# Optimization experiments

Hardware: AMD Instinct MI355X
Metric: run time of the kernel (lower is better)

## Reference

```python
import jax, jax.numpy as jnp
import numpy as np

# Fixed by module source: forward hardcodes a 200x200 BEV grid, dim=128,
# MSDeformAttn(n_levels=1, n_heads=4, n_points=8).
B, Z, X, C, H, P = 2, 200, 200, 128, 4, 8
N = Z * X
D = C // H  # head dim = 32


def setup_inputs() -> dict:
    key = jax.random.key(0)
    ks = jax.random.split(key, 12)
    s = 0.02
    return {
        "query": jax.random.normal(ks[0], (B, N, C), jnp.float32),
        # MSDeformAttn.value_proj
        "Wv": jax.random.normal(ks[1], (C, C), jnp.float32) * s,
        "bv": jnp.zeros((C,), jnp.float32),
        # MSDeformAttn.sampling_offsets (C -> H*1*P*2)
        "Woff": jax.random.normal(ks[2], (C, H * P * 2), jnp.float32) * s,
        "boff": jax.random.normal(ks[3], (H * P * 2,), jnp.float32) * 2.0,
        # MSDeformAttn.attention_weights (C -> H*1*P)
        "Wattn": jax.random.normal(ks[4], (C, H * P), jnp.float32) * s,
        "battn": jnp.zeros((H * P,), jnp.float32),
        # MSDeformAttn.output_proj
        "Wout1": jax.random.normal(ks[5], (C, C), jnp.float32) * s,
        "bout1": jnp.zeros((C,), jnp.float32),
        # VanillaSelfAttention.output_proj
        "Wout2": jax.random.normal(ks[6], (C, C), jnp.float32) * s,
        "bout2": jnp.zeros((C,), jnp.float32),
    }


def _forward(query, Wv, bv, Woff, boff, Wattn, battn, Wout1, bout1, Wout2, bout2):
    # Reference points: normalized centers of the 200x200 grid, order (z, x).
    zc = (jnp.arange(Z, dtype=jnp.float32) + 0.5) / Z
    xc = (jnp.arange(X, dtype=jnp.float32) + 0.5) / X
    ref = jnp.stack(jnp.meshgrid(zc, xc, indexing="ij"), axis=-1).reshape(N, 2)

    # value_proj on input_flatten (== query); split heads, lay out as images.
    value = (query @ Wv + bv).reshape(B, Z, X, H, D)
    value_flat = value.transpose(0, 3, 1, 2, 4).reshape(B * H, Z * X, D)  # (BH, ZX, D)

    # Sampling locations: ref + offsets / offset_normalizer ([W, H] = [200, 200]).
    off = (query @ Woff + boff).reshape(B, N, H, P, 2)
    norm = jnp.array([X, Z], jnp.float32)
    loc = ref[None, :, None, None, :] + off / norm  # (B, N, H, P, 2)

    # Attention weights: softmax over n_levels*n_points (= P here).
    attn = jax.nn.softmax((query @ Wattn + battn).reshape(B, N, H, P), axis=-1)

    # grid_sample convention: grid = 2*loc - 1, grid[...,0]=x (width), align_corners=False.
    grid = 2.0 * loc - 1.0
    ix = ((grid[..., 0] + 1.0) * X - 1.0) * 0.5  # pixel x coords
    iy = ((grid[..., 1] + 1.0) * Z - 1.0) * 0.5  # pixel y coords
    ix = ix.transpose(0, 2, 1, 3).reshape(B * H, N * P)
    iy = iy.transpose(0, 2, 1, 3).reshape(B * H, N * P)

    x0f = jnp.floor(ix); y0f = jnp.floor(iy)
    lx = ix - x0f; ly = iy - y0f
    x0 = x0f.astype(jnp.int32); y0 = y0f.astype(jnp.int32)
    x1 = x0 + 1; y1 = y0 + 1

    def corner(xi, yi, w):
        # zero padding: out-of-bounds corners contribute 0
        valid = (xi >= 0) & (xi < X) & (yi >= 0) & (yi < Z)
        idx = jnp.clip(yi, 0, Z - 1) * X + jnp.clip(xi, 0, X - 1)  # (BH, N*P)
        v = jnp.take_along_axis(value_flat, idx[..., None], axis=1)  # (BH, N*P, D)
        return v * (w * valid.astype(w.dtype))[..., None]

    sampled = (
        corner(x0, y0, (1.0 - lx) * (1.0 - ly))
        + corner(x1, y0, lx * (1.0 - ly))
        + corner(x0, y1, (1.0 - lx) * ly)
        + corner(x1, y1, lx * ly)
    ).reshape(B, H, N, P, D)

    # Weighted reduce over points, merge heads.
    out = jnp.einsum("bhnpd,bnhp->bnhd", sampled, attn).reshape(B, N, C)
    out = out @ Wout1 + bout1  # MSDeformAttn.output_proj
    out = out @ Wout2 + bout2  # VanillaSelfAttention.output_proj
    return out + query  # dropout is identity in eval; residual add


def reference(query, Wv, bv, Woff, boff, Wattn, battn, Wout1, bout1, Wout2, bout2):
    return _forward(query, Wv, bv, Woff, boff, Wattn, battn, Wout1, bout1, Wout2, bout2)
```

## Files before the change

### kernel.cpp

```cpp
#include <hip/hip_runtime.h>
#include <hip/hip_bf16.h>
#include <cstddef>

namespace {
constexpr int B  = 2;
constexpr int Z  = 200;
constexpr int X  = 200;
constexpr int C  = 128;
constexpr int H  = 4;
constexpr int P  = 8;
constexpr int N  = Z * X;
constexpr int BN = B * N;
constexpr int SC = 128;
constexpr int NF_P = 14;
constexpr int NF_O = 8;
constexpr int KS   = 4;

typedef __attribute__((ext_vector_type(8))) short short8;
typedef __attribute__((ext_vector_type(4))) float f32x4;
typedef _Float16 h16x2 __attribute__((ext_vector_type(2)));

__device__ inline ushort f2bf(float x) {
    __hip_bfloat16 h = __float2bfloat16(x);
    return *reinterpret_cast<ushort*>(&h);
}
__device__ inline unsigned packbf(float a, float b) {
    return (unsigned)f2bf(a) | ((unsigned)f2bf(b) << 16);
}
__device__ inline ushort f2h(float x) {
    _Float16 h = (_Float16)x;
    return __builtin_bit_cast(ushort, h);
}
__device__ inline float h1f(ushort u) {
    return (float)__builtin_bit_cast(_Float16, u);
}
__device__ inline float2 h2f2(unsigned u) {
    h16x2 h = __builtin_bit_cast(h16x2, u);
    return make_float2((float)h[0], (float)h[1]);
}
__device__ inline unsigned packh(float a, float b) {
    return (unsigned)f2h(a) | ((unsigned)f2h(b) << 16);
}
__device__ inline h16x2 pkrtz(float a, float b) {
    return __builtin_bit_cast(h16x2, __builtin_amdgcn_cvt_pkrtz(a, b));
}
template <int MASK>
__device__ inline float swzx(float x) {
    constexpr int pat = (MASK << 10) | 0x1F;
    return __int_as_float(__builtin_amdgcn_ds_swizzle(__float_as_int(x), pat));
}
template <int MASK>
__device__ inline h16x2 swzh(h16x2 x) {
    constexpr int pat = (MASK << 10) | 0x1F;
    int t = __builtin_amdgcn_ds_swizzle(__builtin_bit_cast(int, x), pat);
    return __builtin_bit_cast(h16x2, t);
}
}

__global__ __launch_bounds__(256) void vsa_k_prep(
    const float* __restrict__ Wv,    const float* __restrict__ bv,
    const float* __restrict__ Woff,  const float* __restrict__ boff,
    const float* __restrict__ Wattn, const float* __restrict__ battn,
    const float* __restrict__ Wout1, const float* __restrict__ bout1,
    const float* __restrict__ Wout2, const float* __restrict__ bout2,
    ushort* __restrict__ wtp, ushort* __restrict__ wtp2,
    float* __restrict__ biasp, float* __restrict__ bias2)
{
    const int u = blockIdx.x * 256 + threadIdx.x;
    constexpr int NP = KS * NF_P * 64;
    constexpr int NO = KS * NF_O * 64;

    if (u < NP) {
        int ks  = u / (NF_P * 64);
        int rem = u - ks * (NF_P * 64);
        int f = rem >> 6, l = rem & 63;
        int n  = f * 16 + (l & 15);
        int kb = ks * 32 + (l >> 4) * 8;
        float v[8];
        #pragma unroll
        for (int e = 0; e < 8; ++e) {
            int k = kb + e;
            if (n < 128)      v[e] = Wv[k * 128 + n];
            else if (n < 192) v[e] = Woff[k * 64 + (n - 128)];
            else              v[e] = Wattn[k * 32 + (n - 192)];
        }
        unsigned* dst = (unsigned*)(wtp + (size_t)u * 8);
        #pragma unroll
        for (int i = 0; i < 4; ++i) dst[i] = packbf(v[2*i], v[2*i+1]);
    } else if (u < NP + NO) {
        int t   = u - NP;
        int ks  = t / (NF_O * 64);
        int rem = t - ks * (NF_O * 64);
        int f = rem >> 6, l = rem & 63;
        int n  = f * 16 + (l & 15);
        int kb = ks * 32 + (l >> 4) * 8;
        float acc[8] = {0,0,0,0,0,0,0,0};
        for (int j = 0; j < 128; ++j) {
            float w2 = Wout2[j * 128 + n];
            #pragma unroll
            for (int e = 0; e < 8; ++e)
                acc[e] = fmaf(Wout1[(kb + e) * 128 + j], w2, acc[e]);
        }
        unsigned* dst = (unsigned*)(wtp2 + (size_t)t * 8);
        #pragma unroll
        for (int i = 0; i < 4; ++i) dst[i] = packh(acc[2*i], acc[2*i+1]);
    } else if (u < NP + NO + 224) {
        int c = u - NP - NO;
        float bb;
        if (c < 128)      bb = bv[c];
        else if (c < 192) bb = boff[c - 128];
        else              bb = battn[c - 192];
        biasp[c] = bb;
    } else if (u < NP + NO + 224 + 128) {
        int c = u - NP - NO - 224;
        float acc = bout2[c];
        for (int j = 0; j < 128; ++j)
            acc = fmaf(bout1[j], Wout2[j * 128 + c], acc);
        bias2[c] = acc;
    }
}

__global__ __launch_bounds__(256) void vsa_k_proj(
    const float* __restrict__ Q, const ushort* __restrict__ wtp,
    const float* __restrict__ biasp,
    ushort* __restrict__ proj_v16, ushort* __restrict__ proj_s16)
{
    const int lane = threadIdx.x & 63;
    const int wave = blockIdx.x * 4 + (threadIdx.x >> 6);
    const int row0 = wave * 16;
    const int m  = lane & 15;
    const int kg = lane >> 4;

    const float* qp = Q + (size_t)(row0 + m) * 128 + kg * 8;

    f32x4 acc[NF_P];
    #pragma unroll
    for (int f = 0; f < NF_P; ++f) acc[f] = (f32x4){0.f, 0.f, 0.f, 0.f};

    #pragma unroll
    for (int ks = 0; ks < KS; ++ks) {
        float4 a0 = *(const float4*)(qp + ks * 32);
        float4 a1 = *(const float4*)(qp + ks * 32 + 4);
        short8 af;
        af[0] = (short)f2bf(a0.x); af[1] = (short)f2bf(a0.y);
        af[2] = (short)f2bf(a0.z); af[3] = (short)f2bf(a0.w);
        af[4] = (short)f2bf(a1.x); af[5] = (short)f2bf(a1.y);
        af[6] = (short)f2bf(a1.z); af[7] = (short)f2bf(a1.w);
        const short8* wrow = (const short8*)wtp + ks * NF_P * 64 + lane;
        #pragma unroll
        for (int f = 0; f < NF_P; ++f)
            acc[f] = __builtin_amdgcn_mfma_f32_16x16x32_bf16(af, wrow[f * 64], acc[f], 0, 0, 0);
    }

    #pragma unroll
    for (int f = 0; f < 8; ++f) {
        const int col = f * 16 + m;
        const float bb = biasp[col];
        #pragma unroll
        for (int r = 0; r < 4; ++r)
            proj_v16[(size_t)(row0 + kg * 4 + r) * 128 + col] = f2h(acc[f][r] + bb);
    }
    #pragma unroll
    for (int f = 8; f < 12; ++f) {
        const int col = f * 16 + m;
        const float bb = biasp[col];
        const int c  = col - 128;
        const int hp = c >> 1, comp = c & 1;
        #pragma unroll
        for (int r = 0; r < 4; ++r)
            proj_s16[(size_t)(row0 + kg * 4 + r) * SC + hp * 4 + comp] = f2h(acc[f][r] + bb);
    }
    #pragma unroll
    for (int f = 12; f < 14; ++f) {
        const float bb = biasp[f * 16 + m];
        const int hp = (f - 12) * 16 + m;
        #pragma unroll
        for (int r = 0; r < 4; ++r) {
            float v = acc[f][r] + bb;
            float mx = v;
            mx = fmaxf(mx, swzx<1>(mx));
            mx = fmaxf(mx, swzx<2>(mx));
            mx = fmaxf(mx, swzx<4>(mx));
            float ex = __expf(v - mx);
            float sm = ex;
            sm += swzx<1>(sm); sm += swzx<2>(sm); sm += swzx<4>(sm);
            const float wp = ex / sm;
            proj_s16[(size_t)(row0 + kg * 4 + r) * SC + hp * 4 + 2] = f2h(wp);
        }
    }
}

__global__ __launch_bounds__(256) void vsa_k_so(
    const ushort* __restrict__ proj_v16, const ushort* __restrict__ proj_s16,
    const ushort* __restrict__ wtp2, const float* __restrict__ bias2,
    const float* __restrict__ Q, float* __restrict__ out)
{
    __shared__ ushort tmp_lds[16][136];

    const int lane = threadIdx.x & 63;
    const int wv   = threadIdx.x >> 6;
    const int hsub = lane >> 5;
    const int p    = (lane >> 2) & 7;
    const int d8   = lane & 3;

    const int orig = blockIdx.x;
    const int wg   = (orig & 7) * 625 + (orig >> 3);
    const int b    = wg / 2500;
    const int bl0  = (wg - b * 2500) * 16;
    const int i0   = bl0 / 200;
    const int j0   = bl0 - i0 * 200;
    const int bn0  = b * N + bl0;

    const ushort* vb = proj_v16 + (size_t)b * N * 128;

    #pragma unroll
    for (int t = 0; t < 8; ++t) {
        const int unit = t * 4 + wv;
        const int pix  = unit >> 1;
        const int h    = (unit & 1) * 2 + hsub;
        const int jr   = j0 + pix;
        const bool wr  = jr >= 200;
        const int i    = i0 + (wr ? 1 : 0);
        const int j    = wr ? jr - 200 : jr;
        const int bn   = bn0 + pix;

        const uint2 ow = *(const uint2*)(proj_s16 + (size_t)bn * SC + (h * 8 + p) * 4);
        const float2 off = h2f2(ow.x);
        const float  wp  = h1f((ushort)(ow.y & 0xffff));

        const float ixf = (float)i + off.x;
        const float iyf = (float)j + off.y;
        const float x0f = floorf(ixf), y0f = floorf(iyf);
        const float lx = ixf - x0f, ly = iyf - y0f;
        const int x0 = (int)x0f, y0 = (int)y0f;
        const int x1 = x0 + 1,  y1 = y0 + 1;
        const int xc0 = min(max(x0, 0), X - 1), xc1 = min(max(x1, 0), X - 1);
        const int yc0 = min(max(y0, 0), Z - 1), yc1 = min(max(y1, 0), Z - 1);

        const float wx0 = ((unsigned)x0 < (unsigned)X) ? (1.f - lx) : 0.f;
        const float wx1 = ((unsigned)x1 < (unsigned)X) ? lx : 0.f;
        const float wy0 = (((unsigned)y0 < (unsigned)Z) ? (1.f - ly) : 0.f) * wp;
        const float wy1 = (((unsigned)y1 < (unsigned)Z) ? ly : 0.f) * wp;

        const h16x2 w00p = pkrtz(wx0 * wy0, wx0 * wy0);
        const h16x2 w10p = pkrtz(wx1 * wy0, wx1 * wy0);
        const h16x2 w01p = pkrtz(wx0 * wy1, wx0 * wy1);
        const h16x2 w11p = pkrtz(wx1 * wy1, wx1 * wy1);

        const int rb0 = yc0 * X, rb1 = yc1 * X;
        const int hb  = h * 32 + d8 * 8;

        const uint4 c00 = *(const uint4*)(vb + (size_t)(rb0 + xc0) * 128 + hb);
        const uint4 c10 = *(const uint4*)(vb + (size_t)(rb0 + xc1) * 128 + hb);
        const uint4 c01 = *(const uint4*)(vb + (size_t)(rb1 + xc0) * 128 + hb);
        const uint4 c11 = *(const uint4*)(vb + (size_t)(rb1 + xc1) * 128 + hb);

        h16x2 a0 = (h16x2)0, a1 = (h16x2)0, a2 = (h16x2)0, a3 = (h16x2)0;
        #define VSA_ACC(c, wpk) { \
            a0 = __builtin_elementwise_fma(__builtin_bit_cast(h16x2, (c).x), wpk, a0); \
            a1 = __builtin_elementwise_fma(__builtin_bit_cast(h16x2, (c).y), wpk, a1); \
            a2 = __builtin_elementwise_fma(__builtin_bit_cast(h16x2, (c).z), wpk, a2); \
            a3 = __builtin_elementwise_fma(__builtin_bit_cast(h16x2, (c).w), wpk, a3); }
        VSA_ACC(c00, w00p)
        VSA_ACC(c10, w10p)
        VSA_ACC(c01, w01p)
        VSA_ACC(c11, w11p)
        #undef VSA_ACC

        a0 += swzh<4>(a0);  a1 += swzh<4>(a1);  a2 += swzh<4>(a2);  a3 += swzh<4>(a3);
        a0 += swzh<8>(a0);  a1 += swzh<8>(a1);  a2 += swzh<8>(a2);  a3 += swzh<8>(a3);
        a0 += swzh<16>(a0); a1 += swzh<16>(a1); a2 += swzh<16>(a2); a3 += swzh<16>(a3);

        if (p == 0) {
            uint4 o;
            o.x = __builtin_bit_cast(unsigned, a0);
            o.y = __builtin_bit_cast(unsigned, a1);
            o.z = __builtin_bit_cast(unsigned, a2);
            o.w = __builtin_bit_cast(unsigned, a3);
            *(uint4*)(&tmp_lds[pix][h * 32 + d8 * 8]) = o;
        }
    }
    __syncthreads();

    const int m  = lane & 15;
    const int kg = lane >> 4;
    const int f0 = wv * 2;

    f32x4 acc0 = (f32x4){0.f, 0.f, 0.f, 0.f};
    f32x4 acc1 = (f32x4){0.f, 0.f, 0.f, 0.f};
    #pragma unroll
    for (int ks = 0; ks < KS; ++ks) {
        short8 af = *(const short8*)(&tmp_lds[m][ks * 32 + kg * 8]);
        const short8* wrow = (const short8*)wtp2 + ks * NF_O * 64 + lane;
        acc0 = __builtin_amdgcn_mfma_f32_16x16x32_f16(af, wrow[f0 * 64], acc0, 0, 0, 0);
        acc1 = __builtin_amdgcn_mfma_f32_16x16x32_f16(af, wrow[(f0 + 1) * 64], acc1, 0, 0, 0);
    }

    #pragma unroll
    for (int ff = 0; ff < 2; ++ff) {
        const int col = (f0 + ff) * 16 + m;
        const float bb = bias2[col];
        #pragma unroll
        for (int r = 0; r < 4; ++r) {
            const float av = ff ? acc1[r] : acc0[r];
            const size_t gi = (size_t)(bn0 + kg * 4 + r) * 128 + col;
            const float q = __builtin_nontemporal_load(Q + gi);
            __builtin_nontemporal_store(av + bb + q, out + gi);
        }
    }
}

extern "C" void kernel_launch(void* const* d_in, const int* in_sizes, int n_in,
                              void* d_out, int out_size, void* d_ws, size_t ws_size,
                              hipStream_t stream) {
    const float* Q     = (const float*)d_in[0];
    const float* Wv    = (const float*)d_in[1];
    const float* bv    = (const float*)d_in[2];
    const float* Woff  = (const float*)d_in[3];
    const float* boff  = (const float*)d_in[4];
    const float* Wattn = (const float*)d_in[5];
    const float* battn = (const float*)d_in[6];
    const float* Wout1 = (const float*)d_in[7];
    const float* bout1 = (const float*)d_in[8];
    const float* Wout2 = (const float*)d_in[9];
    const float* bout2 = (const float*)d_in[10];
    float* out = (float*)d_out;

    float*  biasp  = (float*)d_ws;
    float*  bias2  = biasp + 224;
    ushort* proj_s16 = (ushort*)(bias2 + 128);
    ushort* proj_v16 = proj_s16 + (size_t)BN * SC;
    ushort* wtp    = proj_v16 + (size_t)BN * 128;
    ushort* wtp2   = wtp + (size_t)KS * NF_P * 64 * 8;

    constexpr int prep_n = KS * NF_P * 64 + KS * NF_O * 64 + 224 + 128;
    vsa_k_prep<<<(prep_n + 255) / 256, 256, 0, stream>>>(
        Wv, bv, Woff, boff, Wattn, battn, Wout1, bout1, Wout2, bout2,
        wtp, wtp2, biasp, bias2);
    vsa_k_proj<<<BN / 64, 256, 0, stream>>>(Q, wtp, biasp, proj_v16, proj_s16);
    vsa_k_so<<<BN / 16, 256, 0, stream>>>(proj_v16, proj_s16, wtp2, bias2, Q, out);
}
```

Baseline: 95.82 us.

## Split fused out-proj weight GEMM into parallel kernel; widen sampling blocks to 512

Result: faster. 92.62 us (-3.3%).

```diff
diff --git a/kernel.cpp b/kernel.cpp
--- a/kernel.cpp
+++ b/kernel.cpp
@@ -57,12 +57,27 @@
 }
 }
 
+__global__ __launch_bounds__(256) void vsa_k_w12(
+    const float* __restrict__ Wout1, const float* __restrict__ bout1,
+    const float* __restrict__ Wout2, const float* __restrict__ bout2,
+    float* __restrict__ w12)
+{
+    const int c = threadIdx.x & 127;
+    const int k = blockIdx.x * 2 + (threadIdx.x >> 7);
+    if (k > 128) return;
+    const float* arow = (k < 128) ? (Wout1 + (size_t)k * 128) : bout1;
+    float acc = (k < 128) ? 0.f : bout2[c];
+    #pragma unroll 4
+    for (int j = 0; j < 128; ++j)
+        acc = fmaf(arow[j], Wout2[(size_t)j * 128 + c], acc);
+    w12[(size_t)k * 128 + c] = acc;
+}
+
 __global__ __launch_bounds__(256) void vsa_k_prep(
     const float* __restrict__ Wv,    const float* __restrict__ bv,
     const float* __restrict__ Woff,  const float* __restrict__ boff,
     const float* __restrict__ Wattn, const float* __restrict__ battn,
-    const float* __restrict__ Wout1, const float* __restrict__ bout1,
-    const float* __restrict__ Wout2, const float* __restrict__ bout2,
+    const float* __restrict__ w12,
     ushort* __restrict__ wtp, ushort* __restrict__ wtp2,
     float* __restrict__ biasp, float* __restrict__ bias2)
 {
@@ -94,16 +109,11 @@
         int f = rem >> 6, l = rem & 63;
         int n  = f * 16 + (l & 15);
         int kb = ks * 32 + (l >> 4) * 8;
-        float acc[8] = {0,0,0,0,0,0,0,0};
-        for (int j = 0; j < 128; ++j) {
-            float w2 = Wout2[j * 128 + n];
-            #pragma unroll
-            for (int e = 0; e < 8; ++e)
-                acc[e] = fmaf(Wout1[(kb + e) * 128 + j], w2, acc[e]);
-        }
         unsigned* dst = (unsigned*)(wtp2 + (size_t)t * 8);
         #pragma unroll
-        for (int i = 0; i < 4; ++i) dst[i] = packh(acc[2*i], acc[2*i+1]);
+        for (int i = 0; i < 4; ++i)
+            dst[i] = packh(w12[(size_t)(kb + 2*i) * 128 + n],
+                           w12[(size_t)(kb + 2*i + 1) * 128 + n]);
     } else if (u < NP + NO + 224) {
         int c = u - NP - NO;
         float bb;
@@ -113,10 +123,7 @@
         biasp[c] = bb;
     } else if (u < NP + NO + 224 + 128) {
         int c = u - NP - NO - 224;
-        float acc = bout2[c];
-        for (int j = 0; j < 128; ++j)
-            acc = fmaf(bout1[j], Wout2[j * 128 + c], acc);
-        bias2[c] = acc;
+        bias2[c] = w12[(size_t)128 * 128 + c];
     }
 }
 
@@ -190,7 +197,7 @@
     }
 }
 
-__global__ __launch_bounds__(256) void vsa_k_so(
+__global__ __launch_bounds__(512) void vsa_k_so(
     const ushort* __restrict__ proj_v16, const ushort* __restrict__ proj_s16,
     const ushort* __restrict__ wtp2, const float* __restrict__ bias2,
     const float* __restrict__ Q, float* __restrict__ out)
@@ -214,8 +221,8 @@
     const ushort* vb = proj_v16 + (size_t)b * N * 128;
 
     #pragma unroll
-    for (int t = 0; t < 8; ++t) {
-        const int unit = t * 4 + wv;
+    for (int t = 0; t < 4; ++t) {
+        const int unit = t * 8 + wv;
         const int pix  = unit >> 1;
         const int h    = (unit & 1) * 2 + hsub;
         const int jr   = j0 + pix;
@@ -284,29 +291,22 @@
 
     const int m  = lane & 15;
     const int kg = lane >> 4;
-    const int f0 = wv * 2;
-
-    f32x4 acc0 = (f32x4){0.f, 0.f, 0.f, 0.f};
-    f32x4 acc1 = (f32x4){0.f, 0.f, 0.f, 0.f};
+
+    f32x4 acc = (f32x4){0.f, 0.f, 0.f, 0.f};
     #pragma unroll
     for (int ks = 0; ks < KS; ++ks) {
         short8 af = *(const short8*)(&tmp_lds[m][ks * 32 + kg * 8]);
         const short8* wrow = (const short8*)wtp2 + ks * NF_O * 64 + lane;
-        acc0 = __builtin_amdgcn_mfma_f32_16x16x32_f16(af, wrow[f0 * 64], acc0, 0, 0, 0);
-        acc1 = __builtin_amdgcn_mfma_f32_16x16x32_f16(af, wrow[(f0 + 1) * 64], acc1, 0, 0, 0);
-    }
-
-    #pragma unroll
-    for (int ff = 0; ff < 2; ++ff) {
-        const int col = (f0 + ff) * 16 + m;
-        const float bb = bias2[col];
-        #pragma unroll
-        for (int r = 0; r < 4; ++r) {
-            const float av = ff ? acc1[r] : acc0[r];
-            const size_t gi = (size_t)(bn0 + kg * 4 + r) * 128 + col;
-            const float q = __builtin_nontemporal_load(Q + gi);
-            __builtin_nontemporal_store(av + bb + q, out + gi);
-        }
+        acc = __builtin_amdgcn_mfma_f32_16x16x32_f16(af, wrow[wv * 64], acc, 0, 0, 0);
+    }
+
+    const int col = wv * 16 + m;
+    const float bb = bias2[col];
+    #pragma unroll
+    for (int r = 0; r < 4; ++r) {
+        const size_t gi = (size_t)(bn0 + kg * 4 + r) * 128 + col;
+        const float q = __builtin_nontemporal_load(Q + gi);
+        __builtin_nontemporal_store(acc[r] + bb + q, out + gi);
     }
 }
 
@@ -328,15 +328,16 @@
 
     float*  biasp  = (float*)d_ws;
     float*  bias2  = biasp + 224;
-    ushort* proj_s16 = (ushort*)(bias2 + 128);
+    float*  w12    = bias2 + 128;
+    ushort* proj_s16 = (ushort*)(w12 + 129 * 128);
     ushort* proj_v16 = proj_s16 + (size_t)BN * SC;
     ushort* wtp    = proj_v16 + (size_t)BN * 128;
     ushort* wtp2   = wtp + (size_t)KS * NF_P * 64 * 8;
 
     constexpr int prep_n = KS * NF_P * 64 + KS * NF_O * 64 + 224 + 128;
+    vsa_k_w12<<<65, 256, 0, stream>>>(Wout1, bout1, Wout2, bout2, w12);
     vsa_k_prep<<<(prep_n + 255) / 256, 256, 0, stream>>>(
-        Wv, bv, Woff, boff, Wattn, battn, Wout1, bout1, Wout2, bout2,
-        wtp, wtp2, biasp, bias2);
+        Wv, bv, Woff, boff, Wattn, battn, w12, wtp, wtp2, biasp, bias2);
     vsa_k_proj<<<BN / 64, 256, 0, stream>>>(Q, wtp, biasp, proj_v16, proj_s16);
-    vsa_k_so<<<BN / 16, 256, 0, stream>>>(proj_v16, proj_s16, wtp2, bias2, Q, out);
-}
+    vsa_k_so<<<BN / 16, 512, 0, stream>>>(proj_v16, proj_s16, wtp2, bias2, Q, out);
+}
```
